# Kernel tuning notes

Hardware: AMD Instinct MI355X
Metric: run time of the kernel (lower is better)

The kernel has to match this reference:

```python
import jax, jax.numpy as jnp
import numpy as np

B, C, H = 4, 64, 48
HEADS, BSWIN = 2, 4
BIG = [3, 6, 12, 24]      # big window edge per scale (cubic)
SMALL = [1, 2, 4, 8]      # small (pool) window edge per scale
NH = 3                    # small windows per big window per dim (= big/small)
L = NH ** 3               # tokens per big window after pooling
CPH = C // (HEADS * BSWIN)  # channels per head per scale = 8


def _rel_pos_index():
    coords = np.stack(np.meshgrid(*([np.arange(NH)] * 3), indexing='ij')).reshape(3, -1)
    rel = coords[:, :, None] - coords[:, None, :] + (NH - 1)
    span = 2 * NH - 1
    return jnp.asarray(rel[0] * span * span + rel[1] * span + rel[2])  # (L, L) int

REL_IDX = _rel_pos_index()


def _interp_matrix(n_in, n_out):
    # 1D linear interpolation matrix, align_corners=True (matches F.interpolate)
    if n_out == n_in:
        return jnp.eye(n_in, dtype=jnp.float32)
    pos = jnp.arange(n_out, dtype=jnp.float32) * (n_in - 1) / (n_out - 1)
    i0 = jnp.clip(jnp.floor(pos).astype(jnp.int32), 0, n_in - 2)
    w = pos - i0.astype(jnp.float32)
    r = jnp.arange(n_out)
    m = jnp.zeros((n_out, n_in), jnp.float32)
    return m.at[r, i0].add(1.0 - w).at[r, i0 + 1].add(w)


def _gather(x):
    # x: (B, C, H, H, H) -> (B, HEADS, sum_N, L, CPH)
    b = x.shape[0]
    x = x.reshape(b, BSWIN, HEADS, CPH, H, H, H)
    parts, Ns = [], []
    for i in range(BSWIN):
        bw, sw = BIG[i], SMALL[i]
        N1 = H // bw
        xi = x[:, i].reshape(b, HEADS, CPH, N1, NH, sw, N1, NH, sw, N1, NH, sw)
        xi = xi.max(axis=(5, 8, 11))  # max-pool each small window
        # (b, head, c, Nh, nh, Nw, nw, Nd, nd) -> b head (Nh Nw Nd) (nh nw nd) c
        xi = xi.transpose(0, 1, 3, 5, 7, 4, 6, 8, 2)
        parts.append(xi.reshape(b, HEADS, N1 ** 3, L, CPH))
        Ns.append(N1)
    return jnp.concatenate(parts, axis=2), Ns


def _scatter(attn, Ns):
    # attn: (B, HEADS, sum_N, L, CPH) -> (B, C, H, H, H)
    b = attn.shape[0]
    outs, idx = [], 0
    for i in range(BSWIN):
        bw, sw = BIG[i], SMALL[i]
        N1 = Ns[i]
        N = N1 ** 3
        o = attn[:, :, idx:idx + N].reshape(b, HEADS, N, NH, NH, NH, CPH)
        M = _interp_matrix(NH, bw)  # trilinear upsample by small window size
        o = jnp.einsum('bhnijkc,pi,qj,rk->bhnpqrc', o, M, M, M)
        o = o.reshape(b, HEADS, N1, N1, N1, bw, bw, bw, CPH)
        # b head Nh Nw Nd wh ww wd c -> b head c (Nh wh) (Nw ww) (Nd wd)
        o = o.transpose(0, 1, 8, 2, 5, 3, 6, 4, 7).reshape(b, HEADS, CPH, H, H, H)
        outs.append(o)
        idx += N
    out = jnp.stack(outs, axis=1)  # b bswin head c h w d
    return out.reshape(b, C, H, H, H)


def _attention(q, k, v, rpb_table):
    c = q.shape[-1]
    scores = jnp.einsum('bhNmc,bhNnc->bhNmn', q, k) / jnp.sqrt(jnp.asarray(c, q.dtype))
    w = jax.nn.softmax(scores, axis=-1)
    bias = rpb_table[REL_IDX].transpose(2, 0, 1)  # (head, L, L), added POST-softmax
    w = w + bias[None, :, None]
    return jnp.einsum('bhNmn,bhNnc->bhNmc', w, v)


def setup_inputs() -> dict:
    key = jax.random.key(0)
    kq, kk, kv, kp = jax.random.split(key, 4)
    shp = (B, C, H, H, H)
    return {
        'query': jax.random.normal(kq, shp, jnp.float32),
        'key': jax.random.normal(kk, shp, jnp.float32),
        'value': jax.random.normal(kv, shp, jnp.float32),
        'rpb_table': jax.random.normal(kp, ((2 * NH - 1) ** 3, HEADS), jnp.float32) * 0.02,
    }


def reference(query, key, value, rpb_table):
    q, Ns = _gather(query)
    k, _ = _gather(key)
    v, _ = _gather(value)
    attn = _attention(q, k, v, rpb_table)
    return _scatter(attn, Ns)
```

## Files before the change

kernel.cpp:

```cpp
#include <hip/hip_runtime.h>


static constexpr long S1 = 4L * 48 * 24 * 24 * 24;
static constexpr long S2 = 4L * 32 * 12 * 12 * 12;
static constexpr long S3 = 4L * 16 * 6 * 6 * 6;

__global__ void pool48_kernel(const float* __restrict__ in0,
                              const float* __restrict__ in1,
                              const float* __restrict__ in2,
                              float* __restrict__ out, long outStride)
{
    constexpr int ZPB = 2;
    constexpr int PLANES = 2 * ZPB;
    constexpr int RSTRIDE = 28;
    __shared__ float xp[PLANES * 48 * RSTRIDE];

    const float* in = blockIdx.y == 0 ? in0 : (blockIdx.y == 1 ? in1 : in2);
    float* o = out + (long)blockIdx.y * outStride;

    int bx = blockIdx.x;
    const int zc = bx % 12; bx /= 12;
    const int c = bx % 48;
    const int b = bx / 48;
    const int zIn0 = zc * PLANES;

    const float* base = in + ((long)b * 64 + 16 + c) * 110592 + (long)zIn0 * 2304;

    for (int i = threadIdx.x; i < PLANES * 48 * 12; i += 256) {
        int p = i / 576;
        int rem = i % 576;
        int r = rem / 12;
        int x4 = rem % 12;
        float4 f = *(const float4*)(base + (long)p * 2304 + r * 48 + 4 * x4);
        float2 m = make_float2(fmaxf(f.x, f.y), fmaxf(f.z, f.w));
        *(float2*)(&xp[(p * 48 + r) * RSTRIDE + 2 * x4]) = m;
    }
    __syncthreads();

    for (int i = threadIdx.x; i < ZPB * 144; i += 256) {
        int zl = i / 144;
        int rem = i % 144;
        int oy = rem / 6;
        int ox4 = rem % 6;
        const float* p0 = &xp[((2 * zl) * 48 + 2 * oy) * RSTRIDE + 4 * ox4];
        const float* p1 = p0 + RSTRIDE;
        const float* p2 = p0 + 48 * RSTRIDE;
        const float* p3 = p2 + RSTRIDE;
        float4 a = *(const float4*)p0;
        float4 bb = *(const float4*)p1;
        float4 cc = *(const float4*)p2;
        float4 d = *(const float4*)p3;
        float4 r4 = make_float4(fmaxf(fmaxf(a.x, bb.x), fmaxf(cc.x, d.x)),
                                fmaxf(fmaxf(a.y, bb.y), fmaxf(cc.y, d.y)),
                                fmaxf(fmaxf(a.z, bb.z), fmaxf(cc.z, d.z)),
                                fmaxf(fmaxf(a.w, bb.w), fmaxf(cc.w, d.w)));
        long oaddr = (((long)b * 48 + c) * 24 + (zc * ZPB + zl)) * 576 + oy * 24 + 4 * ox4;
        *(float4*)(o + oaddr) = r4;
    }
}

template <int OUTW>
__global__ void pool_kernel(const float* __restrict__ in0,
                            const float* __restrict__ in1,
                            const float* __restrict__ in2,
                            float* __restrict__ out, long outStride,
                            int Cin, int chOff, int Cout, int Din, int n)
{
    const float* in = blockIdx.y == 0 ? in0 : (blockIdx.y == 1 ? in1 : in2);
    float* o = out + (long)blockIdx.y * outStride;
    const int Dout = Din >> 1;
    const int QX = Dout / OUTW;
    int idx = blockIdx.x * blockDim.x + threadIdx.x;
    if (idx >= n) return;
    int qx = idx % QX;
    int t = idx / QX;
    int y = t % Dout; t /= Dout;
    int z = t % Dout; t /= Dout;
    int c = t % Cout;
    int b = t / Cout;
    const float* p = in + ((((long)b * Cin + c + chOff) * Din + 2 * z) * Din + 2 * y) * Din
                        + qx * (2 * OUTW);
    const float* rows[4] = { p, p + Din, p + (long)Din * Din, p + (long)Din * Din + Din };

    float v[4][2 * OUTW];
#pragma unroll
    for (int r = 0; r < 4; r++) {
#pragma unroll
        for (int j = 0; j < OUTW / 2; j++) {
            float4 f = *(const float4*)(rows[r] + 4 * j);
            v[r][4 * j + 0] = f.x; v[r][4 * j + 1] = f.y;
            v[r][4 * j + 2] = f.z; v[r][4 * j + 3] = f.w;
        }
    }
    float res[OUTW];
#pragma unroll
    for (int i = 0; i < OUTW; i++) {
        float m0 = fmaxf(v[0][2 * i], v[0][2 * i + 1]);
        float m1 = fmaxf(v[1][2 * i], v[1][2 * i + 1]);
        float m2 = fmaxf(v[2][2 * i], v[2][2 * i + 1]);
        float m3 = fmaxf(v[3][2 * i], v[3][2 * i + 1]);
        res[i] = fmaxf(fmaxf(m0, m1), fmaxf(m2, m3));
    }
    long oaddr = ((((long)b * Cout + c) * Dout + z) * Dout + y) * Dout + qx * OUTW;
    if (OUTW == 4) {
        *(float4*)(o + oaddr) = make_float4(res[0], res[1], res[2], res[3 % OUTW]);
    } else {
        *(float2*)(o + oaddr) = make_float2(res[0], res[1]);
    }
}

template <int S>
__global__ void attn_kernel(const float* __restrict__ qsrc,
                            const float* __restrict__ ksrc,
                            const float* __restrict__ vsrc,
                            const float* __restrict__ rpb,
                            float* __restrict__ attnOut)
{
    constexpr int N1 = (S == 0 ? 16 : S == 1 ? 8 : S == 2 ? 4 : 2);
    constexpr int D  = 3 * N1;
    constexpr int Cs = (S == 0 ? 64 : S == 1 ? 48 : S == 2 ? 32 : 16);
    constexpr int scaleOff = (S == 0 ? 0 : S == 1 ? 4096 : S == 2 ? 4608 : 4672);
    constexpr int VEC = (S == 3 ? 2 : 4);
    constexpr int SEG = 3 * D;
    constexpr int NSEG = 72;
    constexpr int TOTV = NSEG * SEG / VEC;

    __shared__ float tile[N1][3][27][8];
    __shared__ float bias_lds[2][27][27];

    const int b = blockIdx.z;
    const int head = blockIdx.y;
    const int Wz = blockIdx.x / N1;
    const int Wy = blockIdx.x % N1;

    for (int i = threadIdx.x; i < 2 * 729; i += blockDim.x) {
        int h = i / 729;
        int mn = i % 729;
        int m = mn / 27, n = mn % 27;
        int mi = m / 9, mj = (m / 3) % 3, mk = m % 3;
        int ni = n / 9, nj = (n / 3) % 3, nk = n % 3;
        int ridx = (mi - ni + 2) * 25 + (mj - nj + 2) * 5 + (mk - nk + 2);
        bias_lds[h][m][n] = rpb[ridx * 2 + h];
    }

    for (int i = threadIdx.x; i < TOTV; i += blockDim.x) {
        int seg = i / (SEG / VEC);
        int off = (i % (SEG / VEC)) * VEC;
        int tz = seg / 24;
        int rem = seg % 24;
        int cph = rem / 3;
        int zt = rem % 3;
        const float* src = tz == 0 ? qsrc : (tz == 1 ? ksrc : vsrc);
        long base = ((((long)b * Cs + head * 8 + cph) * D + (3 * Wz + zt)) * D + 3 * Wy) * (long)D;
        const float* sp = src + base + off;
        float vals[VEC];
        if (VEC == 4) {
            float4 f = *(const float4*)sp;
            vals[0] = f.x; vals[1] = f.y; vals[2] = f.z; vals[3 % VEC] = f.w;
        } else {
            float2 f = *(const float2*)sp;
            vals[0] = f.x; vals[1] = f.y;
        }
#pragma unroll
        for (int j = 0; j < VEC; j++) {
            int f = off + j;
            int r = f / D;
            int x = f % D;
            tile[x / 3][tz][zt * 9 + r * 3 + (x % 3)][cph] = vals[j];
        }
    }
    __syncthreads();

    const int wx = threadIdx.x >> 5;
    const int lane = threadIdx.x & 31;
    if (lane >= 27) return;
    const int m = lane;

    float qr[8];
#pragma unroll
    for (int c = 0; c < 8; c++) qr[c] = tile[wx][0][m][c];

    float s[27];
    float mx = -1e30f;
#pragma unroll
    for (int n = 0; n < 27; n++) {
        float acc = 0.f;
#pragma unroll
        for (int c = 0; c < 8; c++) acc += qr[c] * tile[wx][1][n][c];
        acc *= 0.35355339059327373f;
        s[n] = acc;
        mx = fmaxf(mx, acc);
    }
    float sum = 0.f;
#pragma unroll
    for (int n = 0; n < 27; n++) {
        s[n] = __expf(s[n] - mx);
        sum += s[n];
    }
    float rs = 1.0f / sum;

    float o[8] = {0, 0, 0, 0, 0, 0, 0, 0};
#pragma unroll
    for (int n = 0; n < 27; n++) {
        float wgt = s[n] * rs + bias_lds[head][m][n];
#pragma unroll
        for (int c = 0; c < 8; c++) o[c] += wgt * tile[wx][2][n][c];
    }

    const int win = (Wz * N1 + Wy) * N1 + wx;
    float* dst = attnOut + (((long)(b * 2 + head) * 4680 + scaleOff + win) * 27 + m) * 8;
    *(float4*)(dst) = make_float4(o[0], o[1], o[2], o[3]);
    *(float4*)(dst + 4) = make_float4(o[4], o[5], o[6], o[7]);
}

template <int S>
__device__ __forceinline__ void scatter_impl(const float* __restrict__ attn,
                                             float* __restrict__ out,
                                             float* lds, int t, int b, int head,
                                             int tid)
{
    constexpr int bw = (S == 0 ? 3 : S == 1 ? 6 : S == 2 ? 12 : 24);
    constexpr int N1 = 48 / bw;
    constexpr int scaleOff = (S == 0 ? 0 : S == 1 ? 4096 : S == 2 ? 4608 : 4672);
    constexpr int CZ = (S == 0 ? 3 : S == 1 ? 3 : 1);
    constexpr int NZC = bw / CZ;
    constexpr int LDSF = N1 * 216;
    constexpr int NF4 = CZ * bw * 8 * 12;

    const int zc = t % NZC; t /= NZC;
    const int Wy = t % N1;
    const int Wz = t / N1;

    const float* src = attn + ((long)(b * 2 + head) * 4680 + scaleOff + (Wz * N1 + Wy) * N1) * 216;
    for (int i = tid; i < LDSF / 4; i += 256)
        *(float4*)(lds + 4 * i) = *(const float4*)(src + 4 * i);
    __syncthreads();

    const float inv = 2.0f / (float)(bw - 1);

    for (int i = tid; i < NF4; i += 256) {
        int x4 = i % 12;
        int t2 = i / 12;
        int cph = t2 % 8; t2 /= 8;
        int y = t2 % bw;
        int zl = t2 / bw;
        int wp = zc * CZ + zl;

        float4 res;
        float* rr = (float*)&res;

        if (S == 0) {
#pragma unroll
            for (int e = 0; e < 4; e++) {
                int r = x4 * 4 + e;
                int Wx = r / 3, wr = r % 3;
                rr[e] = lds[(Wx * 27 + (wp * 3 + y) * 3 + wr) * 8 + cph];
            }
        } else {
            float posp = wp * inv; int i0p = min((int)posp, 1); float fp = posp - (float)i0p;
            float posq = y * inv;  int i0q = min((int)posq, 1); float fq = posq - (float)i0q;
            float wpv[2] = {1.f - fp, fp};
            float wqv[2] = {1.f - fq, fq};
#pragma unroll
            for (int e = 0; e < 4; e++) {
                int r = x4 * 4 + e;
                int Wx = r / bw, wr = r % bw;
                float posr = wr * inv; int i0r = min((int)posr, 1); float fr = posr - (float)i0r;
                float wrv[2] = {1.f - fr, fr};
                const float* basep = lds + Wx * 216 + cph;
                float acc = 0.f;
#pragma unroll
                for (int di = 0; di < 2; di++) {
#pragma unroll
                    for (int dj = 0; dj < 2; dj++) {
#pragma unroll
                        for (int dk = 0; dk < 2; dk++) {
                            int tok = ((i0p + di) * 3 + (i0q + dj)) * 3 + (i0r + dk);
                            acc += wpv[di] * wqv[dj] * wrv[dk] * basep[tok * 8];
                        }
                    }
                }
                rr[e] = acc;
            }
        }

        int z = Wz * bw + wp;
        int Y = Wy * bw + y;
        long oaddr = (((long)(b * 64 + S * 16 + head * 8 + cph) * 48 + z) * 48 + Y) * 48 + x4 * 4;
        *(float4*)(out + oaddr) = res;
    }
}

__global__ void scatter_all(const float* __restrict__ attn, float* __restrict__ out)
{
    __shared__ float lds[16 * 216];
    const int b = blockIdx.z;
    const int head = blockIdx.y;
    const int bx = blockIdx.x;
    const int tid = threadIdx.x;
    if (bx < 256)      scatter_impl<0>(attn, out, lds, bx,       b, head, tid);
    else if (bx < 384) scatter_impl<1>(attn, out, lds, bx - 256, b, head, tid);
    else if (bx < 576) scatter_impl<2>(attn, out, lds, bx - 384, b, head, tid);
    else               scatter_impl<3>(attn, out, lds, bx - 576, b, head, tid);
}

extern "C" void kernel_launch(void* const* d_in, const int* in_sizes, int n_in,
                              void* d_out, int out_size, void* d_ws, size_t ws_size,
                              hipStream_t stream)
{
    const float* q   = (const float*)d_in[0];
    const float* k   = (const float*)d_in[1];
    const float* v   = (const float*)d_in[2];
    const float* rpb = (const float*)d_in[3];
    float* out = (float*)d_out;

    float* ws = (float*)d_ws;
    float* P1 = ws;
    float* P2 = ws + 3 * S1;
    float* P3 = ws + 3 * S1 + 3 * S2;
    float* attn = ws + 3 * S1 + 3 * S2 + 3 * S3;

    pool48_kernel<<<dim3(4 * 48 * 12, 3), 256, 0, stream>>>(q, k, v, P1, S1);

    {
        const int n2 = 4 * 32 * 12 * 12 * 3;
        dim3 g2((n2 + 255) / 256, 3);
        pool_kernel<4><<<g2, 256, 0, stream>>>(P1, P1 + S1, P1 + 2 * S1, P2, S2, 48, 16, 32, 24, n2);

        const int n3 = 4 * 16 * 6 * 6 * 3;
        dim3 g3((n3 + 255) / 256, 3);
        pool_kernel<2><<<g3, 256, 0, stream>>>(P2, P2 + S2, P2 + 2 * S2, P3, S3, 32, 16, 16, 12, n3);
    }

    attn_kernel<0><<<dim3(256, 2, 4), 512, 0, stream>>>(q, k, v, rpb, attn);
    attn_kernel<1><<<dim3(64, 2, 4), 256, 0, stream>>>(P1, P1 + S1, P1 + 2 * S1, rpb, attn);
    attn_kernel<2><<<dim3(16, 2, 4), 128, 0, stream>>>(P2, P2 + S2, P2 + 2 * S2, rpb, attn);
    attn_kernel<3><<<dim3(4, 2, 4), 64, 0, stream>>>(P3, P3 + S3, P3 + 2 * S3, rpb, attn);

    scatter_all<<<dim3(672, 2, 4), 256, 0, stream>>>(attn, out);
}
```

Before: 188.7 us.

## Fuse scale-0 attention with level-1 pooling and write scale-0 output directly

```diff
diff --git a/kernel.cpp b/kernel.cpp
--- a/kernel.cpp
+++ b/kernel.cpp
@@ -5,28 +5,25 @@
 static constexpr long S2 = 4L * 32 * 12 * 12 * 12;
 static constexpr long S3 = 4L * 16 * 6 * 6 * 6;
 
-__global__ void pool48_kernel(const float* __restrict__ in0,
-                              const float* __restrict__ in1,
-                              const float* __restrict__ in2,
-                              float* __restrict__ out, long outStride)
-{
-    constexpr int ZPB = 2;
-    constexpr int PLANES = 2 * ZPB;
+
+__device__ __forceinline__ void pool48_body(int pid, float* xp,
+                                            const float* __restrict__ q,
+                                            const float* __restrict__ k,
+                                            const float* __restrict__ v,
+                                            float* __restrict__ P1)
+{
     constexpr int RSTRIDE = 28;
-    __shared__ float xp[PLANES * 48 * RSTRIDE];
-
-    const float* in = blockIdx.y == 0 ? in0 : (blockIdx.y == 1 ? in1 : in2);
-    float* o = out + (long)blockIdx.y * outStride;
-
-    int bx = blockIdx.x;
-    const int zc = bx % 12; bx /= 12;
-    const int c = bx % 48;
-    const int b = bx / 48;
-    const int zIn0 = zc * PLANES;
-
-    const float* base = in + ((long)b * 64 + 16 + c) * 110592 + (long)zIn0 * 2304;
-
-    for (int i = threadIdx.x; i < PLANES * 48 * 12; i += 256) {
+    const int tz = pid % 3;
+    int rest = pid / 3;
+    const int zc = rest % 12; rest /= 12;
+    const int c = rest % 48;
+    const int b = rest / 48;
+
+    const float* in = tz == 0 ? q : (tz == 1 ? k : v);
+    float* o = P1 + (long)tz * S1;
+    const float* base = in + ((long)b * 64 + 16 + c) * 110592 + (long)(zc * 4) * 2304;
+
+    for (int i = threadIdx.x; i < 4 * 48 * 12; i += 256) {
         int p = i / 576;
         int rem = i % 576;
         int r = rem / 12;
@@ -37,7 +34,7 @@
     }
     __syncthreads();
 
-    for (int i = threadIdx.x; i < ZPB * 144; i += 256) {
+    for (int i = threadIdx.x; i < 288; i += 256) {
         int zl = i / 144;
         int rem = i % 144;
         int oy = rem / 6;
@@ -54,8 +51,143 @@
                                 fmaxf(fmaxf(a.y, bb.y), fmaxf(cc.y, d.y)),
                                 fmaxf(fmaxf(a.z, bb.z), fmaxf(cc.z, d.z)),
                                 fmaxf(fmaxf(a.w, bb.w), fmaxf(cc.w, d.w)));
-        long oaddr = (((long)b * 48 + c) * 24 + (zc * ZPB + zl)) * 576 + oy * 24 + 4 * ox4;
+        long oaddr = (((long)b * 48 + c) * 24 + (zc * 2 + zl)) * 576 + oy * 24 + 4 * ox4;
         *(float4*)(o + oaddr) = r4;
+    }
+}
+
+__device__ __forceinline__ void attn0_body(int aid, float* smem,
+                                           const float* __restrict__ qsrc,
+                                           const float* __restrict__ ksrc,
+                                           const float* __restrict__ vsrc,
+                                           const float* __restrict__ rpb,
+                                           float* __restrict__ out)
+{
+    const int half = aid & 1;
+    int rest = aid >> 1;
+    const int Wy = rest % 16; rest /= 16;
+    const int Wz = rest % 16; rest /= 16;
+    const int head = rest % 2;
+    const int b = rest / 2;
+
+    float* tile = smem;
+    float* bias = smem + 5184;
+    const int tid = threadIdx.x;
+
+    for (int i = tid; i < 2 * 729; i += 256) {
+        int h = i / 729;
+        int mn = i % 729;
+        int m = mn / 27, n = mn % 27;
+        int mi = m / 9, mj = (m / 3) % 3, mk = m % 3;
+        int ni = n / 9, nj = (n / 3) % 3, nk = n % 3;
+        int ridx = (mi - ni + 2) * 25 + (mj - nj + 2) * 5 + (mk - nk + 2);
+        bias[i] = rpb[ridx * 2 + h];
+    }
+
+    for (int i = tid; i < 1296; i += 256) {
+        int seg = i / 6;
+        int off = (i % 6) * 4;
+        int tz = seg / 72;
+        int rem = seg % 72;
+        int cph = rem / 9;
+        int rem2 = rem % 9;
+        int zt = rem2 / 3;
+        int r = rem2 % 3;
+        const float* src = tz == 0 ? qsrc : (tz == 1 ? ksrc : vsrc);
+        long addr = ((((long)b * 64 + head * 8 + cph) * 48 + 3 * Wz + zt) * 48
+                     + 3 * Wy + r) * 48 + half * 24 + off;
+        float4 f = *(const float4*)(src + addr);
+        float vals[4] = {f.x, f.y, f.z, f.w};
+#pragma unroll
+        for (int j = 0; j < 4; j++) {
+            int xl = off + j;
+            int wxl = xl / 3, tk = xl % 3;
+            int tok = zt * 9 + r * 3 + tk;
+            tile[((wxl * 3 + tz) * 27 + tok) * 8 + cph] = vals[j];
+        }
+    }
+    __syncthreads();
+
+    const int wx = tid >> 5;
+    const int lane = tid & 31;
+    if (lane < 27) {
+        const int m = lane;
+        const float* tq = tile + (wx * 3 + 0) * 27 * 8;
+        const float* tk = tile + (wx * 3 + 1) * 27 * 8;
+        const float* tv = tile + (wx * 3 + 2) * 27 * 8;
+        float qr[8];
+#pragma unroll
+        for (int c = 0; c < 8; c++) qr[c] = tq[m * 8 + c];
+
+        float s[27];
+        float mx = -1e30f;
+#pragma unroll
+        for (int n = 0; n < 27; n++) {
+            float acc = 0.f;
+#pragma unroll
+            for (int c = 0; c < 8; c++) acc += qr[c] * tk[n * 8 + c];
+            acc *= 0.35355339059327373f;
+            s[n] = acc;
+            mx = fmaxf(mx, acc);
+        }
+        float sum = 0.f;
+#pragma unroll
+        for (int n = 0; n < 27; n++) {
+            s[n] = __expf(s[n] - mx);
+            sum += s[n];
+        }
+        float rs = 1.0f / sum;
+
+        float o[8] = {0, 0, 0, 0, 0, 0, 0, 0};
+#pragma unroll
+        for (int n = 0; n < 27; n++) {
+            float wgt = s[n] * rs + bias[(head * 27 + m) * 27 + n];
+#pragma unroll
+            for (int c = 0; c < 8; c++) o[c] += wgt * tv[n * 8 + c];
+        }
+        float* to = tile + (wx * 3 + 0) * 27 * 8;
+#pragma unroll
+        for (int c = 0; c < 8; c++) to[m * 8 + c] = o[c];
+    }
+    __syncthreads();
+
+    for (int i = tid; i < 432; i += 256) {
+        int x4i = i % 6;
+        int t2 = i / 6;
+        int cph = t2 % 8; t2 /= 8;
+        int y = t2 % 3;
+        int zl = t2 / 3;
+        float4 res;
+        float* rr = (float*)&res;
+#pragma unroll
+        for (int e = 0; e < 4; e++) {
+            int xl = x4i * 4 + e;
+            int wxl = xl / 3, tk = xl % 3;
+            int tok = zl * 9 + y * 3 + tk;
+            rr[e] = tile[(wxl * 3 + 0) * 27 * 8 + tok * 8 + cph];
+        }
+        int z = 3 * Wz + zl;
+        int Y = 3 * Wy + y;
+        long oaddr = (((long)(b * 64 + head * 8 + cph) * 48 + z) * 48 + Y) * 48
+                     + half * 24 + x4i * 4;
+        *(float4*)(out + oaddr) = res;
+    }
+}
+
+__global__ void fused_pool_attn0(const float* __restrict__ q,
+                                 const float* __restrict__ k,
+                                 const float* __restrict__ v,
+                                 const float* __restrict__ rpb,
+                                 float* __restrict__ P1,
+                                 float* __restrict__ out)
+{
+    __shared__ float smem[6642];
+    const int bx = blockIdx.x;
+    if (bx < 8192 && (bx & 1) == 0) {
+        attn0_body(bx >> 1, smem, q, k, v, rpb, out);
+    } else {
+        int pid = (bx < 8192) ? (bx >> 1) : (bx - 4096);
+        pool48_body(pid, smem, q, k, v, P1);
     }
 }
 
@@ -82,23 +214,23 @@
                         + qx * (2 * OUTW);
     const float* rows[4] = { p, p + Din, p + (long)Din * Din, p + (long)Din * Din + Din };
 
-    float v[4][2 * OUTW];
+    float v2[4][2 * OUTW];
 #pragma unroll
     for (int r = 0; r < 4; r++) {
 #pragma unroll
         for (int j = 0; j < OUTW / 2; j++) {
             float4 f = *(const float4*)(rows[r] + 4 * j);
-            v[r][4 * j + 0] = f.x; v[r][4 * j + 1] = f.y;
-            v[r][4 * j + 2] = f.z; v[r][4 * j + 3] = f.w;
+            v2[r][4 * j + 0] = f.x; v2[r][4 * j + 1] = f.y;
+            v2[r][4 * j + 2] = f.z; v2[r][4 * j + 3] = f.w;
         }
     }
     float res[OUTW];
 #pragma unroll
     for (int i = 0; i < OUTW; i++) {
-        float m0 = fmaxf(v[0][2 * i], v[0][2 * i + 1]);
-        float m1 = fmaxf(v[1][2 * i], v[1][2 * i + 1]);
-        float m2 = fmaxf(v[2][2 * i], v[2][2 * i + 1]);
-        float m3 = fmaxf(v[3][2 * i], v[3][2 * i + 1]);
+        float m0 = fmaxf(v2[0][2 * i], v2[0][2 * i + 1]);
+        float m1 = fmaxf(v2[1][2 * i], v2[1][2 * i + 1]);
+        float m2 = fmaxf(v2[2][2 * i], v2[2][2 * i + 1]);
+        float m3 = fmaxf(v2[3][2 * i], v2[3][2 * i + 1]);
         res[i] = fmaxf(fmaxf(m0, m1), fmaxf(m2, m3));
     }
     long oaddr = ((((long)b * Cout + c) * Dout + z) * Dout + y) * Dout + qx * OUTW;
@@ -116,10 +248,10 @@
                             const float* __restrict__ rpb,
                             float* __restrict__ attnOut)
 {
-    constexpr int N1 = (S == 0 ? 16 : S == 1 ? 8 : S == 2 ? 4 : 2);
+    constexpr int N1 = (S == 1 ? 8 : S == 2 ? 4 : 2);
     constexpr int D  = 3 * N1;
-    constexpr int Cs = (S == 0 ? 64 : S == 1 ? 48 : S == 2 ? 32 : 16);
-    constexpr int scaleOff = (S == 0 ? 0 : S == 1 ? 4096 : S == 2 ? 4608 : 4672);
+    constexpr int Cs = (S == 1 ? 48 : S == 2 ? 32 : 16);
+    constexpr int scaleOff = (S == 1 ? 4096 : S == 2 ? 4608 : 4672);
     constexpr int VEC = (S == 3 ? 2 : 4);
     constexpr int SEG = 3 * D;
     constexpr int NSEG = 72;
@@ -219,10 +351,10 @@
                                              float* lds, int t, int b, int head,
                                              int tid)
 {
-    constexpr int bw = (S == 0 ? 3 : S == 1 ? 6 : S == 2 ? 12 : 24);
+    constexpr int bw = (S == 1 ? 6 : S == 2 ? 12 : 24);
     constexpr int N1 = 48 / bw;
-    constexpr int scaleOff = (S == 0 ? 0 : S == 1 ? 4096 : S == 2 ? 4608 : 4672);
-    constexpr int CZ = (S == 0 ? 3 : S == 1 ? 3 : 1);
+    constexpr int scaleOff = (S == 1 ? 4096 : S == 2 ? 4608 : 4672);
+    constexpr int CZ = (S == 1 ? 3 : 1);
     constexpr int NZC = bw / CZ;
     constexpr int LDSF = N1 * 216;
     constexpr int NF4 = CZ * bw * 8 * 12;
@@ -246,42 +378,32 @@
         int zl = t2 / bw;
         int wp = zc * CZ + zl;
 
+        float posp = wp * inv; int i0p = min((int)posp, 1); float fp = posp - (float)i0p;
+        float posq = y * inv;  int i0q = min((int)posq, 1); float fq = posq - (float)i0q;
+        float wpv[2] = {1.f - fp, fp};
+        float wqv[2] = {1.f - fq, fq};
         float4 res;
         float* rr = (float*)&res;
-
-        if (S == 0) {
-#pragma unroll
-            for (int e = 0; e < 4; e++) {
-                int r = x4 * 4 + e;
-                int Wx = r / 3, wr = r % 3;
-                rr[e] = lds[(Wx * 27 + (wp * 3 + y) * 3 + wr) * 8 + cph];
-            }
-        } else {
-            float posp = wp * inv; int i0p = min((int)posp, 1); float fp = posp - (float)i0p;
-            float posq = y * inv;  int i0q = min((int)posq, 1); float fq = posq - (float)i0q;
-            float wpv[2] = {1.f - fp, fp};
-            float wqv[2] = {1.f - fq, fq};
-#pragma unroll
-            for (int e = 0; e < 4; e++) {
-                int r = x4 * 4 + e;
-                int Wx = r / bw, wr = r % bw;
-                float posr = wr * inv; int i0r = min((int)posr, 1); float fr = posr - (float)i0r;
-                float wrv[2] = {1.f - fr, fr};
-                const float* basep = lds + Wx * 216 + cph;
-                float acc = 0.f;
-#pragma unroll
-                for (int di = 0; di < 2; di++) {
-#pragma unroll
-                    for (int dj = 0; dj < 2; dj++) {
-#pragma unroll
-                        for (int dk = 0; dk < 2; dk++) {
-                            int tok = ((i0p + di) * 3 + (i0q + dj)) * 3 + (i0r + dk);
-                            acc += wpv[di] * wqv[dj] * wrv[dk] * basep[tok * 8];
-                        }
+#pragma unroll
+        for (int e = 0; e < 4; e++) {
+            int r = x4 * 4 + e;
+            int Wx = r / bw, wr = r % bw;
+            float posr = wr * inv; int i0r = min((int)posr, 1); float fr = posr - (float)i0r;
+            float wrv[2] = {1.f - fr, fr};
+            const float* basep = lds + Wx * 216 + cph;
+            float acc = 0.f;
+#pragma unroll
+            for (int di = 0; di < 2; di++) {
+#pragma unroll
+                for (int dj = 0; dj < 2; dj++) {
+#pragma unroll
+                    for (int dk = 0; dk < 2; dk++) {
+                        int tok = ((i0p + di) * 3 + (i0q + dj)) * 3 + (i0r + dk);
+                        acc += wpv[di] * wqv[dj] * wrv[dk] * basep[tok * 8];
                     }
                 }
-                rr[e] = acc;
             }
+            rr[e] = acc;
         }
 
         int z = Wz * bw + wp;
@@ -293,15 +415,14 @@
 
 __global__ void scatter_all(const float* __restrict__ attn, float* __restrict__ out)
 {
-    __shared__ float lds[16 * 216];
+    __shared__ float lds[8 * 216];
     const int b = blockIdx.z;
     const int head = blockIdx.y;
     const int bx = blockIdx.x;
     const int tid = threadIdx.x;
-    if (bx < 256)      scatter_impl<0>(attn, out, lds, bx,       b, head, tid);
-    else if (bx < 384) scatter_impl<1>(attn, out, lds, bx - 256, b, head, tid);
-    else if (bx < 576) scatter_impl<2>(attn, out, lds, bx - 384, b, head, tid);
-    else               scatter_impl<3>(attn, out, lds, bx - 576, b, head, tid);
+    if (bx < 128)      scatter_impl<1>(attn, out, lds, bx,       b, head, tid);
+    else if (bx < 320) scatter_impl<2>(attn, out, lds, bx - 128, b, head, tid);
+    else               scatter_impl<3>(attn, out, lds, bx - 320, b, head, tid);
 }
 
 extern "C" void kernel_launch(void* const* d_in, const int* in_sizes, int n_in,
@@ -320,7 +441,7 @@
     float* P3 = ws + 3 * S1 + 3 * S2;
     float* attn = ws + 3 * S1 + 3 * S2 + 3 * S3;
 
-    pool48_kernel<<<dim3(4 * 48 * 12, 3), 256, 0, stream>>>(q, k, v, P1, S1);
+    fused_pool_attn0<<<11008, 256, 0, stream>>>(q, k, v, rpb, P1, out);
 
     {
         const int n2 = 4 * 32 * 12 * 12 * 3;
@@ -332,10 +453,9 @@
         pool_kernel<2><<<g3, 256, 0, stream>>>(P2, P2 + S2, P2 + 2 * S2, P3, S3, 32, 16, 16, 12, n3);
     }
 
-    attn_kernel<0><<<dim3(256, 2, 4), 512, 0, stream>>>(q, k, v, rpb, attn);
     attn_kernel<1><<<dim3(64, 2, 4), 256, 0, stream>>>(P1, P1 + S1, P1 + 2 * S1, rpb, attn);
     attn_kernel<2><<<dim3(16, 2, 4), 128, 0, stream>>>(P2, P2 + S2, P2 + 2 * S2, rpb, attn);
     attn_kernel<3><<<dim3(4, 2, 4), 64, 0, stream>>>(P3, P3 + S3, P3 + 2 * S3, rpb, attn);
 
-    scatter_all<<<dim3(672, 2, 4), 256, 0, stream>>>(attn, out);
-}
+    scatter_all<<<dim3(416, 2, 4), 256, 0, stream>>>(attn, out);
+}
```

Result: no change. 187.8 us (-0.5%).
